# Performance work log

Measured on AMD Instinct MI355X. Metric: run time of the kernel, lower is better.

Reference implementation:

```python
import jax, jax.numpy as jnp
from jax import lax
import numpy as np

EPS = 1e-6

def layer_norm(x, scale, bias):
    mu = jnp.mean(x, axis=-1, keepdims=True)
    var = jnp.var(x, axis=-1, keepdims=True)
    y = (x - mu) * lax.rsqrt(var + EPS)
    if scale is not None:
        y = y * scale
    if bias is not None:
        y = y + bias
    return y

def mha(keys, values, queries, mask, head_count):
    # keys/values: [B, K, E]; queries: [B, Q, E]; mask: [B, K] (1 = attend)
    B, Q, E = queries.shape
    d = E // head_count
    q = queries.reshape(B, Q, head_count, d) / jnp.asarray(d ** 0.5, queries.dtype)
    k = keys.reshape(B, -1, head_count, d)
    v = values.reshape(B, -1, head_count, d)
    bias = (1.0 - mask.astype(q.dtype)) * -1e12  # [B, K]
    w = jnp.einsum('bqhc,bkhc->bhqk', q, k) + bias[:, None, None, :]
    w = jax.nn.softmax(w, axis=-1)
    out = jnp.einsum('bhqk,bkhc->bqhc', w, v)
    return out.reshape(B, Q, E)

def setup_inputs() -> dict:
    key = jax.random.key(0)
    ks = jax.random.split(key, 16)
    B, T, E, G, I = 64, 64, 2048, 4096, 256
    s = 0.02
    inp = {
        'decoder_state': jax.random.normal(ks[0], (B, 1, E), jnp.float32),
        'encoder_state': jax.random.normal(ks[1], (B, T, E), jnp.float32),
        'attention_state': jnp.zeros((2 * B, I, E), jnp.float32),
        'attention_mask': jnp.ones((B, T), jnp.int32),
        'token_index': 100,
        # params
        'ln_pre_sa_b': jnp.zeros((E,), jnp.float32),
        'q_sa': s * jax.random.normal(ks[2], (E, E), jnp.float32),
        'k_sa': s * jax.random.normal(ks[3], (E, E), jnp.float32),
        'v_sa': s * jax.random.normal(ks[4], (E, E), jnp.float32),
        'o_sa': s * jax.random.normal(ks[5], (E, E), jnp.float32),
        'ln_sa_s': jnp.ones((E,), jnp.float32),
        'ln_sa_b': jnp.zeros((E,), jnp.float32),
        'ln_pre_ca_b': jnp.zeros((E,), jnp.float32),
        'q_ca': s * jax.random.normal(ks[6], (E, E), jnp.float32),
        'k_ca': s * jax.random.normal(ks[7], (E, E), jnp.float32),
        'v_ca': s * jax.random.normal(ks[8], (E, E), jnp.float32),
        'o_ca': s * jax.random.normal(ks[9], (E, E), jnp.float32),
        'ln_ca_s': jnp.ones((E,), jnp.float32),
        'ln_ca_b': jnp.zeros((E,), jnp.float32),
        'glu_ln0_b': jnp.zeros((E,), jnp.float32),
        'fc0_w': s * jax.random.normal(ks[10], (E, G), jnp.float32),
        'fc1_w': s * jax.random.normal(ks[11], (E, G), jnp.float32),
        'glu_ln1_s': jnp.ones((G,), jnp.float32),
        'glu_ln1_b': jnp.zeros((G,), jnp.float32),
        'fc2_w': s * jax.random.normal(ks[12], (G, E), jnp.float32),
    }
    return inp

IMAGE_TOKEN_COUNT = 256
HEAD_COUNT = 32

def reference(decoder_state, encoder_state, attention_state,
              ln_pre_sa_b, q_sa, k_sa, v_sa, o_sa, ln_sa_s, ln_sa_b,
              ln_pre_ca_b, q_ca, k_ca, v_ca, o_ca, ln_ca_s, ln_ca_b,
              glu_ln0_b, fc0_w, fc1_w, glu_ln1_s, glu_ln1_b, fc2_w,
              attention_mask, token_index):
    B = decoder_state.shape[0]
    # --- self attention (pre-norm, KV cache update) ---
    residual = decoder_state
    x = layer_norm(decoder_state, None, ln_pre_sa_b)
    self_mask = jnp.tile(jnp.arange(IMAGE_TOKEN_COUNT) < token_index + 1, (B, 1))
    keys = x @ k_sa
    values = x @ v_sa
    queries = x @ q_sa
    attention_state = lax.dynamic_update_slice(
        attention_state, jnp.concatenate([keys, values]).astype(jnp.float32),
        (0, token_index, 0))
    cached_k = attention_state[:B]
    cached_v = attention_state[B:]
    x = (mha(cached_k, cached_v, queries, self_mask, HEAD_COUNT) @ o_sa).astype(decoder_state.dtype)
    x = layer_norm(x, ln_sa_s, ln_sa_b)
    decoder_state = residual + x
    # --- cross attention ---
    residual = decoder_state
    x = layer_norm(decoder_state, None, ln_pre_ca_b)
    ek = encoder_state @ k_ca
    ev = encoder_state @ v_ca
    q = x @ q_ca
    x = mha(ek, ev, q, attention_mask, HEAD_COUNT) @ o_ca
    x = layer_norm(x, ln_ca_s, ln_ca_b)
    decoder_state = residual + x
    # --- GLU FFN ---
    residual = decoder_state
    z = layer_norm(decoder_state, None, glu_ln0_b)
    w = jax.nn.gelu(z @ fc0_w, approximate=False)
    v = z @ fc1_w
    z = layer_norm(w * v, glu_ln1_s, glu_ln1_b) @ fc2_w
    decoder_state = residual + z
    return decoder_state, attention_state
```

## Files before the change

### kernel.cpp

```cpp
#include <hip/hip_runtime.h>

#define Bb   64
#define Ee   2048
#define Tt   64
#define Gg   4096
#define Ii   256
#define Hh   32
#define Dd   64

using f32x4_t  = __attribute__((ext_vector_type(4))) float;
using bf16x8_t = __attribute__((ext_vector_type(8))) __bf16;

__device__ __forceinline__ unsigned short f2bf(float f) {
  unsigned u = __float_as_uint(f);
  u += 0x7FFFu + ((u >> 16) & 1u);
  return (unsigned short)(u >> 16);
}
__device__ __forceinline__ float ldkv(float v) { return v; }
__device__ __forceinline__ float ldkv(unsigned short v) {
  return __uint_as_float(((unsigned)v) << 16);
}
__device__ __forceinline__ float gelu_f(float x) {
  return 0.5f * x * (1.0f + erff(x * 0.70710678118654752f));
}

template <typename T> __device__ __forceinline__ float4 ld4(const T* p);
template <> __device__ __forceinline__ float4 ld4<float>(const float* p) {
  return *(const float4*)p;
}
template <> __device__ __forceinline__ float4 ld4<unsigned short>(const unsigned short* p) {
  ushort4 u = *(const ushort4*)p;
  return make_float4(ldkv(u.x), ldkv(u.y), ldkv(u.z), ldkv(u.w));
}

__global__ void copy_state_k(const float4* __restrict__ src, float4* __restrict__ dst,
                             const float4* __restrict__ kb, const float4* __restrict__ vb,
                             const int* __restrict__ tokp) {
  const int t = *tokp;
  const long n4 = (long)128 * Ii * (Ee / 4);
  long i = (long)blockIdx.x * blockDim.x + threadIdx.x;
  const long stride = (long)gridDim.x * blockDim.x;
  for (; i < n4; i += stride) {
    long row = i >> 9;
    int tt = (int)(row & (Ii - 1));
    float4 v;
    if (tt == t) {
      int bh  = (int)(row >> 8);
      int col = (int)(i & 511);
      const float4* s = (bh < Bb) ? kb : vb;
      v = s[(long)(bh & (Bb - 1)) * (Ee / 4) + col];
    } else {
      v = src[i];
    }
    dst[i] = v;
  }
}

__global__ void conv_bf16_k(const float4* __restrict__ in, unsigned short* __restrict__ out, long n4) {
  long i = (long)blockIdx.x * blockDim.x + threadIdx.x;
  long stride = (long)gridDim.x * blockDim.x;
  for (; i < n4; i += stride) {
    float4 f = in[i];
    ushort4 u;
    u.x = f2bf(f.x); u.y = f2bf(f.y); u.z = f2bf(f.z); u.w = f2bf(f.w);
    *(ushort4*)(out + i * 4) = u;
  }
}

__global__ void transpose_bf16_k(const float* __restrict__ W, unsigned short* __restrict__ Wt,
                                 int K, int N) {
  __shared__ unsigned short tile[64][65];
  int k0 = blockIdx.x * 64, n0 = blockIdx.y * 64;
  int c = threadIdx.x & 63;
  int r4 = threadIdx.x >> 6;
  #pragma unroll
  for (int i = 0; i < 16; i++) {
    int r = r4 + i * 4;
    tile[r][c] = f2bf(W[(long)(k0 + r) * N + n0 + c]);
  }
  __syncthreads();
  #pragma unroll
  for (int i = 0; i < 16; i++) {
    int r = r4 + i * 4;
    Wt[(long)(n0 + r) * K + k0 + c] = tile[c][r];
  }
}

template <bool GELU, bool HAS_SCALE, bool HAS_RES, bool DUAL>
__global__ void ln_k(const float4* __restrict__ in1, const float4* __restrict__ in2,
                     const float* __restrict__ scale, const float* __restrict__ bias,
                     const float4* __restrict__ res,
                     float4* __restrict__ out1, float4* __restrict__ out2) {
  const int row = blockIdx.x, tid = threadIdx.x;
  const int C = blockDim.x * 4;
  const long base = (long)row * blockDim.x + tid;

  float4 p = in1[base];
  if (GELU) {
    float4 vv = in2[base];
    p.x = gelu_f(p.x) * vv.x; p.y = gelu_f(p.y) * vv.y;
    p.z = gelu_f(p.z) * vv.z; p.w = gelu_f(p.w) * vv.w;
  }
  float s  = p.x + p.y + p.z + p.w;
  float s2 = p.x * p.x + p.y * p.y + p.z * p.z + p.w * p.w;

  __shared__ float rs[16], rs2[16];
  int lane = tid & 63, w = tid >> 6;
  #pragma unroll
  for (int o = 32; o; o >>= 1) { s += __shfl_down(s, o, 64); s2 += __shfl_down(s2, o, 64); }
  if (lane == 0) { rs[w] = s; rs2[w] = s2; }
  __syncthreads();
  if (tid == 0) {
    float ts = 0.f, ts2 = 0.f;
    int nw = blockDim.x >> 6;
    for (int i = 0; i < nw; i++) { ts += rs[i]; ts2 += rs2[i]; }
    float mu = ts / C;
    float var = ts2 / C - mu * mu;
    rs[0]  = mu;
    rs2[0] = rsqrtf(var + 1e-6f);
  }
  __syncthreads();
  const float mu = rs[0], rstd = rs2[0];

  float4 o;
  o.x = (p.x - mu) * rstd; o.y = (p.y - mu) * rstd;
  o.z = (p.z - mu) * rstd; o.w = (p.w - mu) * rstd;
  if (HAS_SCALE) {
    float4 sc4 = ((const float4*)scale)[tid];
    o.x *= sc4.x; o.y *= sc4.y; o.z *= sc4.z; o.w *= sc4.w;
  }
  float4 b4 = ((const float4*)bias)[tid];
  o.x += b4.x; o.y += b4.y; o.z += b4.z; o.w += b4.w;
  if (HAS_RES) {
    float4 r4 = res[base];
    o.x += r4.x; o.y += r4.y; o.z += r4.z; o.w += r4.w;
  }
  out1[base] = o;
  if (DUAL) out2[base] = o;
}

template <int NW>
__global__ __launch_bounds__(256)
void proj_k(const float* __restrict__ X,
            const float* __restrict__ W0, const float* __restrict__ W1,
            const float* __restrict__ W2,
            float* __restrict__ Y0, float* __restrict__ Y1, float* __restrict__ Y2,
            int K, int N) {
  __shared__ float Xs[64 * 64];
  const int nq = threadIdx.x & 31;
  const int m0 = (threadIdx.x >> 5) * 8;
  const int n  = blockIdx.x * 128 + nq * 4;
  const int kbase = blockIdx.y * 128;

  f32x4_t acc[NW][8];
  #pragma unroll
  for (int wsel = 0; wsel < NW; wsel++)
    #pragma unroll
    for (int i = 0; i < 8; i++) acc[wsel][i] = (f32x4_t){0.f, 0.f, 0.f, 0.f};

  for (int k0 = kbase; k0 < kbase + 128; k0 += 64) {
    __syncthreads();
    #pragma unroll
    for (int j = 0; j < 16; j++) {
      int e = threadIdx.x + j * 256;
      Xs[e] = X[(long)(e >> 6) * K + k0 + (e & 63)];
    }
    __syncthreads();
    #pragma unroll 4
    for (int kk = 0; kk < 64; kk++) {
      const long wrow = (long)(k0 + kk) * N + n;
      f32x4_t w4[NW];
      w4[0] = *(const f32x4_t*)(W0 + wrow);
      if (NW > 1) w4[1] = *(const f32x4_t*)(W1 + wrow);
      if (NW > 2) w4[2] = *(const f32x4_t*)(W2 + wrow);
      #pragma unroll
      for (int i = 0; i < 8; i++) {
        float xm = Xs[(m0 + i) * 64 + kk];
        #pragma unroll
        for (int wsel = 0; wsel < NW; wsel++) acc[wsel][i] += xm * w4[wsel];
      }
    }
  }
  float* Ys[3] = {Y0, Y1, Y2};
  #pragma unroll
  for (int wsel = 0; wsel < NW; wsel++) {
    #pragma unroll
    for (int i = 0; i < 8; i++) {
      float* yp = Ys[wsel] + (long)(m0 + i) * N + n;
      unsafeAtomicAdd(yp + 0, acc[wsel][i][0]);
      unsafeAtomicAdd(yp + 1, acc[wsel][i][1]);
      unsafeAtomicAdd(yp + 2, acc[wsel][i][2]);
      unsafeAtomicAdd(yp + 3, acc[wsel][i][3]);
    }
  }
}

template <typename KVT>
__global__ void attn_k(const float* __restrict__ Q, const KVT* __restrict__ Kc,
                       const KVT* __restrict__ Vc, float* __restrict__ O,
                       const int* __restrict__ tokp, const int* __restrict__ maskp,
                       int L, long bstride, float scale) {
  const int b = blockIdx.x, h = blockIdx.y;
  const int lane = threadIdx.x;
  __shared__ float sc[256];
  const float* qp = Q + (long)b * Ee + h * Dd;
  const int n = tokp ? (*tokp + 1) : L;

  float mx = -3.0e38f;
  for (int pos = lane; pos < n; pos += 64) {
    bool valid = maskp ? (maskp[(long)b * L + pos] != 0) : true;
    float s = -1.0e30f;
    if (valid) {
      const KVT* kr = Kc + (long)b * bstride + (long)pos * Ee + h * Dd;
      float acc = 0.f;
      #pragma unroll
      for (int j = 0; j < 16; j++) {
        float4 kv = ld4(kr + j * 4);
        acc += qp[j*4+0]*kv.x + qp[j*4+1]*kv.y + qp[j*4+2]*kv.z + qp[j*4+3]*kv.w;
      }
      s = acc * scale;
    }
    sc[pos] = s;
    mx = fmaxf(mx, s);
  }
  __syncthreads();
  #pragma unroll
  for (int o = 32; o; o >>= 1) mx = fmaxf(mx, __shfl_down(mx, o, 64));
  mx = __shfl(mx, 0, 64);

  float sum = 0.f;
  for (int pos = lane; pos < n; pos += 64) {
    float e = expf(sc[pos] - mx);
    sc[pos] = e;
    sum += e;
  }
  __syncthreads();
  #pragma unroll
  for (int o = 32; o; o >>= 1) sum += __shfl_down(sum, o, 64);
  sum = __shfl(sum, 0, 64);
  const float inv = 1.0f / sum;

  const KVT* vbase = Vc + (long)b * bstride + h * Dd + lane;
  float acc = 0.f;
  int pos = 0;
  for (; pos + 8 <= n; pos += 8) {
    #pragma unroll
    for (int u = 0; u < 8; u++)
      acc += sc[pos + u] * ldkv(vbase[(long)(pos + u) * Ee]);
  }
  for (; pos < n; pos++) acc += sc[pos] * ldkv(vbase[(long)pos * Ee]);
  O[(long)b * Ee + h * Dd + lane] = acc * inv;
}

__global__ __launch_bounds__(256)
void gemm_bf16_k(const unsigned short* __restrict__ A, const unsigned short* __restrict__ Bt,
                 unsigned short* __restrict__ C, int M, int N, int K) {
  __shared__ unsigned short As[128 * 32];
  __shared__ unsigned short Bs[128 * 32];
  const int m0 = blockIdx.x * 128;
  const int n0 = blockIdx.y * 128;
  const int tid  = threadIdx.x;
  const int lane = tid & 63;
  const int wave = tid >> 6;
  const int wm = (wave >> 1) * 64;
  const int wn = (wave & 1) * 64;
  const int fr = lane & 15;
  const int fq = lane >> 4;

  const int r0 = tid >> 2;
  const int g0 = tid & 3;
  const int so1 = r0 * 32 + ((g0 ^ ((r0 >> 1) & 3)) * 8);
  const int so2 = so1 + 64 * 32;

  f32x4_t acc[4][4];
  const f32x4_t zero = {0.f, 0.f, 0.f, 0.f};
  #pragma unroll
  for (int i = 0; i < 4; i++)
    #pragma unroll
    for (int j = 0; j < 4; j++) acc[i][j] = zero;

  const long aR1 = (long)(m0 + r0) * K;
  const long aR2 = (long)(m0 + r0 + 64) * K;
  const long bR1 = (long)(n0 + r0) * K;
  const long bR2 = (long)(n0 + r0 + 64) * K;

  for (int k0 = 0; k0 < K; k0 += 32) {
    uint4 va1 = *(const uint4*)(A  + aR1 + k0 + g0 * 8);
    uint4 va2 = *(const uint4*)(A  + aR2 + k0 + g0 * 8);
    uint4 vb1 = *(const uint4*)(Bt + bR1 + k0 + g0 * 8);
    uint4 vb2 = *(const uint4*)(Bt + bR2 + k0 + g0 * 8);
    __syncthreads();
    *(uint4*)(As + so1) = va1;
    *(uint4*)(As + so2) = va2;
    *(uint4*)(Bs + so1) = vb1;
    *(uint4*)(Bs + so2) = vb2;
    __syncthreads();

    bf16x8_t af[4], bb[4];
    #pragma unroll
    for (int ms = 0; ms < 4; ms++) {
      int row = wm + ms * 16 + fr;
      af[ms] = __builtin_bit_cast(bf16x8_t,
               *(const uint4*)(As + row * 32 + ((fq ^ ((row >> 1) & 3)) * 8)));
    }
    #pragma unroll
    for (int ns = 0; ns < 4; ns++) {
      int row = wn + ns * 16 + fr;
      bb[ns] = __builtin_bit_cast(bf16x8_t,
               *(const uint4*)(Bs + row * 32 + ((fq ^ ((row >> 1) & 3)) * 8)));
    }
    #pragma unroll
    for (int ms = 0; ms < 4; ms++)
      #pragma unroll
      for (int ns = 0; ns < 4; ns++)
        acc[ms][ns] = __builtin_amdgcn_mfma_f32_16x16x32_bf16(af[ms], bb[ns], acc[ms][ns], 0, 0, 0);
  }

  #pragma unroll
  for (int ms = 0; ms < 4; ms++) {
    #pragma unroll
    for (int ns = 0; ns < 4; ns++) {
      int row = m0 + wm + ms * 16 + fq * 4;
      int col = n0 + wn + ns * 16 + fr;
      #pragma unroll
      for (int r = 0; r < 4; r++)
        C[(long)(row + r) * N + col] = f2bf(acc[ms][ns][r]);
    }
  }
}

extern "C" void kernel_launch(void* const* d_in, const int* in_sizes, int n_in,
                              void* d_out, int out_size, void* d_ws, size_t ws_size,
                              hipStream_t stream) {
  const float* dec    = (const float*)d_in[0];
  const float* enc    = (const float*)d_in[1];
  const float* astate = (const float*)d_in[2];
  const int*   amask  = (const int*)d_in[3];
  const int*   tokp   = (const int*)d_in[4];
  const float* ln_pre_sa_b = (const float*)d_in[5];
  const float* q_sa = (const float*)d_in[6];
  const float* k_sa = (const float*)d_in[7];
  const float* v_sa = (const float*)d_in[8];
  const float* o_sa = (const float*)d_in[9];
  const float* ln_sa_s = (const float*)d_in[10];
  const float* ln_sa_b = (const float*)d_in[11];
  const float* ln_pre_ca_b = (const float*)d_in[12];
  const float* q_ca = (const float*)d_in[13];
  const float* k_ca = (const float*)d_in[14];
  const float* v_ca = (const float*)d_in[15];
  const float* o_ca = (const float*)d_in[16];
  const float* ln_ca_s = (const float*)d_in[17];
  const float* ln_ca_b = (const float*)d_in[18];
  const float* glu_ln0_b = (const float*)d_in[19];
  const float* fc0 = (const float*)d_in[20];
  const float* fc1 = (const float*)d_in[21];
  const float* glu_ln1_s = (const float*)d_in[22];
  const float* glu_ln1_b = (const float*)d_in[23];
  const float* fc2 = (const float*)d_in[24];

  float* out_dec   = (float*)d_out;
  float* out_state = out_dec + (long)Bb * Ee;

  float* qb  = (float*)d_ws;
  float* kb  = qb  + 131072;
  float* vb  = kb  + 131072;
  float* ob  = vb  + 131072;
  float* q2  = ob  + 131072;
  float* ob2 = q2  + 131072;
  float* w0  = ob2 + 131072;
  float* v1  = w0  + 262144;
  size_t zero_bytes = (6L * 131072 + 2L * 262144) * 4;
  float* x1  = v1  + 262144;
  float* ab  = x1  + 131072;
  float* ds2 = ab  + 131072;
  float* x3  = ds2 + 131072;
  float* cb  = x3  + 131072;
  float* ds3 = cb  + 131072;
  float* zb  = ds3 + 131072;
  float* wvn = zb  + 131072;
  unsigned short* ebf = (unsigned short*)(wvn + 262144);
  unsigned short* kt  = ebf + 8388608;
  unsigned short* vt  = kt  + 4194304;
  unsigned short* ekb = vt  + 4194304;
  unsigned short* evb = ekb + 8388608;

  hipMemsetAsync(d_ws, 0, zero_bytes, stream);

  conv_bf16_k<<<2048, 256, 0, stream>>>((const float4*)enc, ebf, (long)Bb * Tt * Ee / 4);
  transpose_bf16_k<<<dim3(32, 32), 256, 0, stream>>>(k_ca, kt, Ee, Ee);
  transpose_bf16_k<<<dim3(32, 32), 256, 0, stream>>>(v_ca, vt, Ee, Ee);
  gemm_bf16_k<<<dim3(32, 16), 256, 0, stream>>>(ebf, kt, ekb, 4096, Ee, Ee);
  gemm_bf16_k<<<dim3(32, 16), 256, 0, stream>>>(ebf, vt, evb, 4096, Ee, Ee);

  ln_k<false,false,false,false><<<Bb, 512, 0, stream>>>(
      (const float4*)dec, nullptr, nullptr, ln_pre_sa_b, nullptr, (float4*)x1, nullptr);
  proj_k<3><<<dim3(16, 16), 256, 0, stream>>>(x1, q_sa, k_sa, v_sa, qb, kb, vb, Ee, Ee);
  copy_state_k<<<4096, 256, 0, stream>>>((const float4*)astate, (float4*)out_state,
                                         (const float4*)kb, (const float4*)vb, tokp);
  attn_k<float><<<dim3(Bb, Hh), 64, 0, stream>>>(qb, out_state,
      out_state + (long)Bb * Ii * Ee, ab, tokp, nullptr, Ii, (long)Ii * Ee, 0.125f);
  proj_k<1><<<dim3(16, 16), 256, 0, stream>>>(ab, o_sa, nullptr, nullptr, ob, nullptr, nullptr, Ee, Ee);
  ln_k<false,true,true,false><<<Bb, 512, 0, stream>>>(
      (const float4*)ob, nullptr, ln_sa_s, ln_sa_b, (const float4*)dec, (float4*)ds2, nullptr);

  ln_k<false,false,false,false><<<Bb, 512, 0, stream>>>(
      (const float4*)ds2, nullptr, nullptr, ln_pre_ca_b, nullptr, (float4*)x3, nullptr);
  proj_k<1><<<dim3(16, 16), 256, 0, stream>>>(x3, q_ca, nullptr, nullptr, q2, nullptr, nullptr, Ee, Ee);
  attn_k<unsigned short><<<dim3(Bb, Hh), 64, 0, stream>>>(q2, ekb, evb, cb,
      nullptr, amask, Tt, (long)Tt * Ee, 0.125f);
  proj_k<1><<<dim3(16, 16), 256, 0, stream>>>(cb, o_ca, nullptr, nullptr, ob2, nullptr, nullptr, Ee, Ee);
  ln_k<false,true,true,true><<<Bb, 512, 0, stream>>>(
      (const float4*)ob2, nullptr, ln_ca_s, ln_ca_b, (const float4*)ds2,
      (float4*)ds3, (float4*)out_dec);

  ln_k<false,false,false,false><<<Bb, 512, 0, stream>>>(
      (const float4*)ds3, nullptr, nullptr, glu_ln0_b, nullptr, (float4*)zb, nullptr);
  proj_k<2><<<dim3(32, 16), 256, 0, stream>>>(zb, fc0, fc1, nullptr, w0, v1, nullptr, Ee, Gg);
  ln_k<true,true,false,false><<<Bb, 1024, 0, stream>>>(
      (const float4*)w0, (const float4*)v1, glu_ln1_s, glu_ln1_b, nullptr, (float4*)wvn, nullptr);
  proj_k<1><<<dim3(16, 32), 256, 0, stream>>>(wvn, fc2, nullptr, nullptr, out_dec, nullptr, nullptr, Gg, Ee);
}
```

Measured before the change: 1.314 ms.

## Replace split-K atomic accumulation with partial buffers and a separate reduction kernel

The projection kernels now write each K-slice's partial results with plain vector stores into a scratch arena, instead of issuing scalar float atomics into the output. A new reduce kernel then sums the slices into the destination buffers, and the last projection adds onto the existing residual in out_dec. This removes the workspace memset and the atomic contention. In exchange it adds one extra launch per projection and a large partial-sum buffer that must be written and read back, which costs extra memory traffic.

After: 1.067 ms. -18.8%, faster.

```diff
diff --git a/kernel.cpp b/kernel.cpp
--- a/kernel.cpp
+++ b/kernel.cpp
@@ -144,8 +144,7 @@
 void proj_k(const float* __restrict__ X,
             const float* __restrict__ W0, const float* __restrict__ W1,
             const float* __restrict__ W2,
-            float* __restrict__ Y0, float* __restrict__ Y1, float* __restrict__ Y2,
-            int K, int N) {
+            float* __restrict__ P, int K, int N) {
   __shared__ float Xs[64 * 64];
   const int nq = threadIdx.x & 31;
   const int m0 = (threadIdx.x >> 5) * 8;
@@ -181,18 +180,27 @@
       }
     }
   }
-  float* Ys[3] = {Y0, Y1, Y2};
+  float* base = P + (long)blockIdx.y * ((long)NW * 64 * N);
   #pragma unroll
   for (int wsel = 0; wsel < NW; wsel++) {
     #pragma unroll
     for (int i = 0; i < 8; i++) {
-      float* yp = Ys[wsel] + (long)(m0 + i) * N + n;
-      unsafeAtomicAdd(yp + 0, acc[wsel][i][0]);
-      unsafeAtomicAdd(yp + 1, acc[wsel][i][1]);
-      unsafeAtomicAdd(yp + 2, acc[wsel][i][2]);
-      unsafeAtomicAdd(yp + 3, acc[wsel][i][3]);
-    }
-  }
+      *(f32x4_t*)(base + ((long)wsel * 64 + m0 + i) * N + n) = acc[wsel][i];
+    }
+  }
+}
+
+template <bool ACCUM>
+__global__ void reduce_k(const float4* __restrict__ P, float4* __restrict__ Y,
+                         int KB, long n4) {
+  long i = (long)blockIdx.x * blockDim.x + threadIdx.x;
+  if (i >= n4) return;
+  float4 s = ACCUM ? Y[i] : make_float4(0.f, 0.f, 0.f, 0.f);
+  for (int k = 0; k < KB; k++) {
+    float4 p = P[(long)k * n4 + i];
+    s.x += p.x; s.y += p.y; s.z += p.z; s.w += p.w;
+  }
+  Y[i] = s;
 }
 
 template <typename KVT>
@@ -369,7 +377,6 @@
   float* ob2 = q2  + 131072;
   float* w0  = ob2 + 131072;
   float* v1  = w0  + 262144;
-  size_t zero_bytes = (6L * 131072 + 2L * 262144) * 4;
   float* x1  = v1  + 262144;
   float* ab  = x1  + 131072;
   float* ds2 = ab  + 131072;
@@ -383,8 +390,7 @@
   unsigned short* vt  = kt  + 4194304;
   unsigned short* ekb = vt  + 4194304;
   unsigned short* evb = ekb + 8388608;
-
-  hipMemsetAsync(d_ws, 0, zero_bytes, stream);
+  float* arena = (float*)(evb + 8388608);
 
   conv_bf16_k<<<2048, 256, 0, stream>>>((const float4*)enc, ebf, (long)Bb * Tt * Ee / 4);
   transpose_bf16_k<<<dim3(32, 32), 256, 0, stream>>>(k_ca, kt, Ee, Ee);
@@ -394,29 +400,35 @@
 
   ln_k<false,false,false,false><<<Bb, 512, 0, stream>>>(
       (const float4*)dec, nullptr, nullptr, ln_pre_sa_b, nullptr, (float4*)x1, nullptr);
-  proj_k<3><<<dim3(16, 16), 256, 0, stream>>>(x1, q_sa, k_sa, v_sa, qb, kb, vb, Ee, Ee);
+  proj_k<3><<<dim3(16, 16), 256, 0, stream>>>(x1, q_sa, k_sa, v_sa, arena, Ee, Ee);
+  reduce_k<false><<<384, 256, 0, stream>>>((const float4*)arena, (float4*)qb, 16, 98304);
   copy_state_k<<<4096, 256, 0, stream>>>((const float4*)astate, (float4*)out_state,
                                          (const float4*)kb, (const float4*)vb, tokp);
   attn_k<float><<<dim3(Bb, Hh), 64, 0, stream>>>(qb, out_state,
       out_state + (long)Bb * Ii * Ee, ab, tokp, nullptr, Ii, (long)Ii * Ee, 0.125f);
-  proj_k<1><<<dim3(16, 16), 256, 0, stream>>>(ab, o_sa, nullptr, nullptr, ob, nullptr, nullptr, Ee, Ee);
+  proj_k<1><<<dim3(16, 16), 256, 0, stream>>>(ab, o_sa, nullptr, nullptr, arena, Ee, Ee);
+  reduce_k<false><<<128, 256, 0, stream>>>((const float4*)arena, (float4*)ob, 16, 32768);
   ln_k<false,true,true,false><<<Bb, 512, 0, stream>>>(
       (const float4*)ob, nullptr, ln_sa_s, ln_sa_b, (const float4*)dec, (float4*)ds2, nullptr);
 
   ln_k<false,false,false,false><<<Bb, 512, 0, stream>>>(
       (const float4*)ds2, nullptr, nullptr, ln_pre_ca_b, nullptr, (float4*)x3, nullptr);
-  proj_k<1><<<dim3(16, 16), 256, 0, stream>>>(x3, q_ca, nullptr, nullptr, q2, nullptr, nullptr, Ee, Ee);
+  proj_k<1><<<dim3(16, 16), 256, 0, stream>>>(x3, q_ca, nullptr, nullptr, arena, Ee, Ee);
+  reduce_k<false><<<128, 256, 0, stream>>>((const float4*)arena, (float4*)q2, 16, 32768);
   attn_k<unsigned short><<<dim3(Bb, Hh), 64, 0, stream>>>(q2, ekb, evb, cb,
       nullptr, amask, Tt, (long)Tt * Ee, 0.125f);
-  proj_k<1><<<dim3(16, 16), 256, 0, stream>>>(cb, o_ca, nullptr, nullptr, ob2, nullptr, nullptr, Ee, Ee);
+  proj_k<1><<<dim3(16, 16), 256, 0, stream>>>(cb, o_ca, nullptr, nullptr, arena, Ee, Ee);
+  reduce_k<false><<<128, 256, 0, stream>>>((const float4*)arena, (float4*)ob2, 16, 32768);
   ln_k<false,true,true,true><<<Bb, 512, 0, stream>>>(
       (const float4*)ob2, nullptr, ln_ca_s, ln_ca_b, (const float4*)ds2,
       (float4*)ds3, (float4*)out_dec);
 
   ln_k<false,false,false,false><<<Bb, 512, 0, stream>>>(
       (const float4*)ds3, nullptr, nullptr, glu_ln0_b, nullptr, (float4*)zb, nullptr);
-  proj_k<2><<<dim3(32, 16), 256, 0, stream>>>(zb, fc0, fc1, nullptr, w0, v1, nullptr, Ee, Gg);
+  proj_k<2><<<dim3(32, 16), 256, 0, stream>>>(zb, fc0, fc1, nullptr, arena, Ee, Gg);
+  reduce_k<false><<<512, 256, 0, stream>>>((const float4*)arena, (float4*)w0, 16, 131072);
   ln_k<true,true,false,false><<<Bb, 1024, 0, stream>>>(
       (const float4*)w0, (const float4*)v1, glu_ln1_s, glu_ln1_b, nullptr, (float4*)wvn, nullptr);
-  proj_k<1><<<dim3(16, 32), 256, 0, stream>>>(wvn, fc2, nullptr, nullptr, out_dec, nullptr, nullptr, Gg, Ee);
-}
+  proj_k<1><<<dim3(16, 32), 256, 0, stream>>>(wvn, fc2, nullptr, nullptr, arena, Gg, Ee);
+  reduce_k<true><<<128, 256, 0, stream>>>((const float4*)arena, (float4*)out_dec, 32, 32768);
+}
```
